# Kernel tuning notes

Measured on AMD Instinct MI355X. Metric: run time of the kernel, lower is better.

## Reference

```python
import jax, jax.numpy as jnp
import numpy as np

N_NODES = 50000
N_EDGES = 800000
D_FEAT = 128
D_HID = 500


def setup_inputs() -> dict:
    key = jax.random.key(0)
    k1, k2, k3, k4 = jax.random.split(key, 4)
    x = jax.random.normal(k1, (N_NODES, D_FEAT), dtype=jnp.float32)
    edge_index = jax.random.randint(k2, (2, N_EDGES), 0, N_NODES, dtype=jnp.int64)
    # Glorot-ish init for weights, zeros for bias (PyG GCNConv default)
    W1 = jax.random.normal(k3, (D_FEAT, D_HID), dtype=jnp.float32) / np.sqrt(D_FEAT)
    b1 = jnp.zeros((D_HID,), dtype=jnp.float32)
    W2 = jax.random.normal(k4, (D_HID, 1), dtype=jnp.float32) / np.sqrt(D_HID)
    b2 = jnp.zeros((1,), dtype=jnp.float32)
    return {"x": x, "edge_index": edge_index, "W1": W1, "b1": b1, "W2": W2, "b2": b2}


def gcn_conv(x, W, b, src, dst, n_nodes):
    """PyG GCNConv: linear transform, add self-loops, symmetric norm, scatter-add, bias."""
    h = x @ W  # [N, out]
    loops = jnp.arange(n_nodes, dtype=src.dtype)
    s = jnp.concatenate([src, loops])  # [E+N]
    d = jnp.concatenate([dst, loops])
    deg = jnp.zeros((n_nodes,), dtype=h.dtype).at[d].add(1.0)
    dinv = jnp.where(deg > 0, jax.lax.rsqrt(deg), 0.0)
    norm = dinv[s] * dinv[d]  # [E+N]
    msg = h[s] * norm[:, None]  # [E+N, out] -- dominant memory traffic
    out = jax.ops.segment_sum(msg, d, num_segments=n_nodes)
    return out + b


def reference(x, edge_index, W1, b1, W2, b2):
    src, dst = edge_index[0], edge_index[1]
    n = x.shape[0]
    h = gcn_conv(x, W1, b1, src, dst, n)
    h = jax.nn.relu(h)
    # F.dropout(training=self.training): identity in eval mode
    out = gcn_conv(h, W2, b2, src, dst, n)
    return out
```

## Files before the change

kernel.cpp:

```cpp
#include <hip/hip_runtime.h>


#define N_NODES 50000
#define N_EDGES 800000
#define D_FEAT  128
#define D_HID   500
#define NTILES  3125
#define BHIST   64
#define EPB     12500
#define CONVB   392
#define CSTRIDE 64

typedef __bf16 bf16x8 __attribute__((ext_vector_type(8)));
typedef float  f32x4  __attribute__((ext_vector_type(4)));

static __device__ inline unsigned int f2bf(float f) {
    unsigned int u = __float_as_uint(f);
    return (u + 0x7fffu + ((u >> 16) & 1u)) >> 16;
}
static __device__ inline float bf_lo(unsigned int u) { return __uint_as_float(u << 16); }
static __device__ inline float bf_hi(unsigned int u) { return __uint_as_float(u & 0xffff0000u); }

static __device__ inline void add8(float* acc, uint4 u) {
    acc[0] += bf_lo(u.x);
    acc[1] += bf_hi(u.x);
    acc[2] += bf_lo(u.y);
    acc[3] += bf_hi(u.y);
    acc[4] += bf_lo(u.z);
    acc[5] += bf_hi(u.z);
    acc[6] += bf_lo(u.w);
    acc[7] += bf_hi(u.w);
}

__global__ __launch_bounds__(1024) void k_hist(const int* __restrict__ dst,
                                               const float* __restrict__ W1,
                                               const float* __restrict__ b1,
                                               const float* __restrict__ W2,
                                               unsigned char* __restrict__ coff,
                                               unsigned char* __restrict__ lrank,
                                               unsigned short* __restrict__ b_pk,
                                               float* __restrict__ b1p,
                                               float* __restrict__ w2p) {
    __shared__ unsigned int hist[N_NODES / 4];
    const int b = blockIdx.x, tid = threadIdx.x;
    if (b < BHIST) {
        for (int w = tid; w < N_NODES / 4; w += 1024) hist[w] = 0u;
        __syncthreads();
        const int base = b * EPB;
        for (int i = tid * 4; i < EPB; i += 4096) {
            int4 d4 = *(const int4*)&dst[base + i];
            unsigned int s0 = (unsigned int)(d4.x & 3) * 8u;
            unsigned int s1 = (unsigned int)(d4.y & 3) * 8u;
            unsigned int s2 = (unsigned int)(d4.z & 3) * 8u;
            unsigned int s3 = (unsigned int)(d4.w & 3) * 8u;
            unsigned int r0 = atomicAdd(&hist[d4.x >> 2], 1u << s0);
            unsigned int r1 = atomicAdd(&hist[d4.y >> 2], 1u << s1);
            unsigned int r2 = atomicAdd(&hist[d4.z >> 2], 1u << s2);
            unsigned int r3 = atomicAdd(&hist[d4.w >> 2], 1u << s3);
            uchar4 lr;
            lr.x = (unsigned char)((r0 >> s0) & 0xffu);
            lr.y = (unsigned char)((r1 >> s1) & 0xffu);
            lr.z = (unsigned char)((r2 >> s2) & 0xffu);
            lr.w = (unsigned char)((r3 >> s3) & 0xffu);
            *(uchar4*)&lrank[base + i] = lr;
        }
        __syncthreads();
        unsigned int* crow = (unsigned int*)coff + (size_t)b * (N_NODES / 4);
        for (int w = tid; w < N_NODES / 4; w += 1024) crow[w] = hist[w];
    } else if (b < BHIST + 8) {
        int idx  = (b - BHIST) * 1024 + tid;
        int lane = idx & 63;
        int slot = idx >> 6;
        int t    = slot >> 2;
        int ks   = slot & 3;
        int quad = lane >> 4;
        int n    = t * 16 + (lane & 15);
        unsigned int us[8];
#pragma unroll
        for (int j = 0; j < 8; j++) {
            int k = ks * 32 + quad * 8 + j;
            float v = (n < D_HID) ? W1[(size_t)k * D_HID + n] : 0.f;
            us[j] = f2bf(v);
        }
        uint4 p;
        p.x = us[0] | (us[1] << 16);
        p.y = us[2] | (us[3] << 16);
        p.z = us[4] | (us[5] << 16);
        p.w = us[6] | (us[7] << 16);
        ((uint4*)b_pk)[idx] = p;
    } else {
        if (tid < 512) {
            b1p[tid] = (tid < D_HID) ? b1[tid] : 0.f;
            w2p[tid] = (tid < D_HID) ? W2[tid] : 0.f;
        }
    }
}

__global__ __launch_bounds__(256) void k_scan(unsigned int* __restrict__ coffw,
                                              int* __restrict__ deg) {
    const int t = blockIdx.x * 256 + threadIdx.x;
    if (t >= N_NODES / 4) return;
    unsigned int run0 = 0, run1 = 0, run2 = 0, run3 = 0;
#pragma unroll 8
    for (int b = 0; b < BHIST; b++) {
        size_t idx = (size_t)b * (N_NODES / 4) + t;
        unsigned int c = coffw[idx];
        coffw[idx] = run0 | (run1 << 8) | (run2 << 16) | (run3 << 24);
        run0 += c & 0xffu;
        run1 += (c >> 8) & 0xffu;
        run2 += (c >> 16) & 0xffu;
        run3 += (c >> 24) & 0xffu;
    }
    int4 d;
    d.x = (int)run0; d.y = (int)run1; d.z = (int)run2; d.w = (int)run3;
    *(int4*)&deg[t * 4] = d;
}

__global__ __launch_bounds__(1024) void k_fill(const int* __restrict__ src,
                                               const int* __restrict__ dst,
                                               const unsigned char* __restrict__ coff,
                                               const unsigned char* __restrict__ lrank,
                                               const int* __restrict__ deg,
                                               const float* __restrict__ x,
                                               unsigned short* __restrict__ csrp,
                                               uint2* __restrict__ xd) {
    const int b = blockIdx.x, tid = threadIdx.x;
    if (b < BHIST) {
        __shared__ unsigned char lcoff[N_NODES];
        const unsigned int* crow =
            (const unsigned int*)coff + (size_t)b * (N_NODES / 4);
        for (int w = tid; w < N_NODES / 4; w += 1024)
            ((unsigned int*)lcoff)[w] = crow[w];
        __syncthreads();
        const int base = b * EPB;
        for (int i = tid * 4; i < EPB; i += 4096) {
            int4 s4 = *(const int4*)&src[base + i];
            int4 d4 = *(const int4*)&dst[base + i];
            uchar4 lr = *(const uchar4*)&lrank[base + i];
            int r0 = (int)lcoff[d4.x] + (int)lr.x;
            int r1 = (int)lcoff[d4.y] + (int)lr.y;
            int r2 = (int)lcoff[d4.z] + (int)lr.z;
            int r3 = (int)lcoff[d4.w] + (int)lr.w;
            if (r0 < CSTRIDE) csrp[d4.x * CSTRIDE + r0] = (unsigned short)s4.x;
            if (r1 < CSTRIDE) csrp[d4.y * CSTRIDE + r1] = (unsigned short)s4.y;
            if (r2 < CSTRIDE) csrp[d4.z * CSTRIDE + r2] = (unsigned short)s4.z;
            if (r3 < CSTRIDE) csrp[d4.w * CSTRIDE + r3] = (unsigned short)s4.w;
        }
    } else {
        int gid = (b - BHIST) * 1024 + tid;
        for (int i = gid; i < N_NODES * D_FEAT / 4; i += CONVB * 1024) {
            float dv = rsqrtf((float)(deg[i >> 5] + 1));
            float4 v = ((const float4*)x)[i];
            uint2 o;
            o.x = f2bf(dv * v.x) | (f2bf(dv * v.y) << 16);
            o.y = f2bf(dv * v.z) | (f2bf(dv * v.w) << 16);
            xd[i] = o;
        }
    }
}

__global__ __launch_bounds__(256, 8) void k_gcn1(const uint4* __restrict__ xd4,
                                                 const unsigned short* __restrict__ csrp,
                                                 const int* __restrict__ deg,
                                                 const unsigned short* __restrict__ b_pk,
                                                 const float* __restrict__ b1p,
                                                 const float* __restrict__ w2p,
                                                 float* __restrict__ zd) {
    __shared__ unsigned short A[16][136];
    __shared__ float red[4][16];
    const int t = threadIdx.x;
    const int node0 = blockIdx.x * 16;
    const int wv = t >> 6, lane = t & 63;
    const int q = lane >> 4, p = lane & 15;

    {
        const int n = wv * 4 + q;
        const int node = node0 + n;
        int dg = deg[node];
        uint4 su = xd4[(size_t)node * 16 + p];
        if (dg > CSTRIDE) dg = CSTRIDE;
        const int base = node * CSTRIDE;
        float acc[8];
#pragma unroll
        for (int j = 0; j < 8; j++) acc[j] = 0.f;

        int e = 0;
        for (; e + 4 <= dg; e += 4) {
            ushort4 s4 = *(const ushort4*)&csrp[base + e];
            uint4 u0 = xd4[(size_t)s4.x * 16 + p];
            uint4 u1 = xd4[(size_t)s4.y * 16 + p];
            uint4 u2 = xd4[(size_t)s4.z * 16 + p];
            uint4 u3 = xd4[(size_t)s4.w * 16 + p];
            add8(acc, u0);
            add8(acc, u1);
            add8(acc, u2);
            add8(acc, u3);
        }
        for (; e < dg; e++) {
            int s = csrp[base + e];
            uint4 u = xd4[(size_t)s * 16 + p];
            add8(acc, u);
        }

        const float di = rsqrtf((float)(dg + 1));
        uint4 o;
        o.x = f2bf(di * (acc[0] + bf_lo(su.x))) |
              (f2bf(di * (acc[1] + bf_hi(su.x))) << 16);
        o.y = f2bf(di * (acc[2] + bf_lo(su.y))) |
              (f2bf(di * (acc[3] + bf_hi(su.y))) << 16);
        o.z = f2bf(di * (acc[4] + bf_lo(su.z))) |
              (f2bf(di * (acc[5] + bf_hi(su.z))) << 16);
        o.w = f2bf(di * (acc[6] + bf_lo(su.w))) |
              (f2bf(di * (acc[7] + bf_hi(su.w))) << 16);
        *(uint4*)&A[n][p * 8] = o;
    }
    __syncthreads();

    bf16x8 afr[4];
#pragma unroll
    for (int ks = 0; ks < 4; ks++)
        afr[ks] = *(const bf16x8*)&A[p][ks * 32 + q * 8];

    const bf16x8* __restrict__ bpk = (const bf16x8*)b_pk;
    f32x4 acc[8];
#pragma unroll
    for (int tt = 0; tt < 8; tt++) acc[tt] = (f32x4){0.f, 0.f, 0.f, 0.f};
#pragma unroll
    for (int tt = 0; tt < 8; tt++) {
        const int tile_n = wv * 8 + tt;
#pragma unroll
        for (int ks = 0; ks < 4; ks++) {
            bf16x8 bfr = bpk[(size_t)(tile_n * 4 + ks) * 64 + lane];
            acc[tt] = __builtin_amdgcn_mfma_f32_16x16x32_bf16(afr[ks], bfr, acc[tt], 0, 0, 0);
        }
    }

    float zp[4] = {0.f, 0.f, 0.f, 0.f};
#pragma unroll
    for (int tt = 0; tt < 8; tt++) {
        const int c = (wv * 8 + tt) * 16 + p;
        const float b1v = b1p[c];
        const float w2v = w2p[c];
#pragma unroll
        for (int r = 0; r < 4; r++)
            zp[r] += fmaxf(acc[tt][r] + b1v, 0.f) * w2v;
    }
#pragma unroll
    for (int off = 1; off < 16; off <<= 1) {
#pragma unroll
        for (int r = 0; r < 4; r++) zp[r] += __shfl_xor(zp[r], off);
    }
    if (p == 0) {
#pragma unroll
        for (int r = 0; r < 4; r++) red[wv][q * 4 + r] = zp[r];
    }
    __syncthreads();
    if (t < 16) {
        int node = node0 + t;
        float zz = red[0][t] + red[1][t] + red[2][t] + red[3][t];
        zd[node] = rsqrtf((float)(deg[node] + 1)) * zz;
    }
}

__global__ __launch_bounds__(256) void k_gz(const unsigned short* __restrict__ csrp,
                                            const int* __restrict__ deg,
                                            const float* __restrict__ zd,
                                            const float* __restrict__ b2,
                                            float* __restrict__ out) {
    const int node = blockIdx.x * 16 + (threadIdx.x >> 4);
    const int l = threadIdx.x & 15;
    int dg = deg[node];
    if (dg > CSTRIDE) dg = CSTRIDE;
    const int base = node * CSTRIDE;
    float s = 0.f;
    for (int e = l; e < dg; e += 16) s += zd[csrp[base + e]];
#pragma unroll
    for (int off = 1; off < 16; off <<= 1) s += __shfl_xor(s, off);
    if (l == 0) {
        float di = rsqrtf((float)(dg + 1));
        out[node] = di * (s + zd[node]) + b2[0];
    }
}

extern "C" void kernel_launch(void* const* d_in, const int* in_sizes, int n_in,
                              void* d_out, int out_size, void* d_ws, size_t ws_size,
                              hipStream_t stream) {
    const float* x  = (const float*)d_in[0];
    const int*   ei = (const int*)d_in[1];
    const float* W1 = (const float*)d_in[2];
    const float* b1 = (const float*)d_in[3];
    const float* W2 = (const float*)d_in[4];
    const float* b2 = (const float*)d_in[5];
    float* out = (float*)d_out;

    const int* src = ei;
    const int* dst = ei + N_EDGES;

    uint2* xd            = (uint2*)d_ws;
    unsigned short* b_pk = (unsigned short*)(xd + 1600000);
    float* b1p    = (float*)(b_pk + 65536);
    float* w2p    = b1p + 512;
    float* zd     = w2p + 512;
    int* deg      = (int*)(zd + N_NODES);
    unsigned char* coff  = (unsigned char*)(deg + N_NODES);
    unsigned char* lrank = coff + (size_t)BHIST * N_NODES;
    unsigned short* csrp = (unsigned short*)(lrank + N_EDGES);

    k_hist<<<BHIST + 9, 1024, 0, stream>>>(dst, W1, b1, W2, coff, lrank,
                                           b_pk, b1p, w2p);
    k_scan<<<(N_NODES / 4 + 255) / 256, 256, 0, stream>>>((unsigned int*)coff, deg);
    k_fill<<<BHIST + CONVB, 1024, 0, stream>>>(src, dst, coff, lrank, deg, x,
                                               csrp, xd);
    k_gcn1<<<NTILES, 256, 0, stream>>>((const uint4*)xd, csrp, deg,
                                       b_pk, b1p, w2p, zd);
    k_gz  <<<NTILES, 256, 0, stream>>>(csrp, deg, zd, b2, out);
}
```

Before: 154.0 us.

## Replace fixed-stride CSR with compact per-group row offsets and split fill blocks

```diff
diff --git a/kernel.cpp b/kernel.cpp
--- a/kernel.cpp
+++ b/kernel.cpp
@@ -8,8 +8,13 @@
 #define NTILES  3125
 #define BHIST   64
 #define EPB     12500
+#define SPLIT   5
+#define SB      (BHIST * SPLIT)
+#define EPSB    (EPB / SPLIT)
 #define CONVB   392
-#define CSTRIDE 64
+#define NGROUP  49
+#define GSTRIDE 24576
+#define CSRE_SLOTS (NGROUP * GSTRIDE)
 
 typedef __bf16 bf16x8 __attribute__((ext_vector_type(8)));
 typedef float  f32x4  __attribute__((ext_vector_type(4)));
@@ -97,57 +102,84 @@
 }
 
 __global__ __launch_bounds__(256) void k_scan(unsigned int* __restrict__ coffw,
-                                              int* __restrict__ deg) {
-    const int t = blockIdx.x * 256 + threadIdx.x;
-    if (t >= N_NODES / 4) return;
+                                              int* __restrict__ deg,
+                                              unsigned int* __restrict__ rstart4) {
+    __shared__ unsigned int ps[256];
+    const int g = blockIdx.x, tid = threadIdx.x;
+    const int idx = g * 256 + tid;
+    const bool live = idx < N_NODES / 4;
     unsigned int run0 = 0, run1 = 0, run2 = 0, run3 = 0;
+    if (live) {
 #pragma unroll 8
-    for (int b = 0; b < BHIST; b++) {
-        size_t idx = (size_t)b * (N_NODES / 4) + t;
-        unsigned int c = coffw[idx];
-        coffw[idx] = run0 | (run1 << 8) | (run2 << 16) | (run3 << 24);
-        run0 += c & 0xffu;
-        run1 += (c >> 8) & 0xffu;
-        run2 += (c >> 16) & 0xffu;
-        run3 += (c >> 24) & 0xffu;
-    }
-    int4 d;
-    d.x = (int)run0; d.y = (int)run1; d.z = (int)run2; d.w = (int)run3;
-    *(int4*)&deg[t * 4] = d;
+        for (int b = 0; b < BHIST; b++) {
+            size_t i = (size_t)b * (N_NODES / 4) + idx;
+            unsigned int c = coffw[i];
+            coffw[i] = run0 | (run1 << 8) | (run2 << 16) | (run3 << 24);
+            run0 += c & 0xffu;
+            run1 += (c >> 8) & 0xffu;
+            run2 += (c >> 16) & 0xffu;
+            run3 += (c >> 24) & 0xffu;
+        }
+        int4 d;
+        d.x = (int)run0; d.y = (int)run1; d.z = (int)run2; d.w = (int)run3;
+        *(int4*)&deg[idx * 4] = d;
+    }
+    unsigned int s0 = (run0 + 3u) & ~3u, s1 = (run1 + 3u) & ~3u;
+    unsigned int s2 = (run2 + 3u) & ~3u, s3 = (run3 + 3u) & ~3u;
+    unsigned int tot = live ? (s0 + s1 + s2 + s3) : 0u;
+    ps[tid] = tot;
+    __syncthreads();
+    for (int off = 1; off < 256; off <<= 1) {
+        unsigned int v = (tid >= off) ? ps[tid - off] : 0u;
+        __syncthreads();
+        ps[tid] += v;
+        __syncthreads();
+    }
+    if (live) {
+        unsigned int base = (unsigned int)g * GSTRIDE + (ps[tid] - tot);
+        uint4 r;
+        r.x = base;
+        r.y = base + s0;
+        r.z = base + s0 + s1;
+        r.w = base + s0 + s1 + s2;
+        *(uint4*)&rstart4[idx * 4] = r;
+    }
 }
 
 __global__ __launch_bounds__(1024) void k_fill(const int* __restrict__ src,
                                                const int* __restrict__ dst,
                                                const unsigned char* __restrict__ coff,
                                                const unsigned char* __restrict__ lrank,
+                                               const unsigned int* __restrict__ rstart4,
                                                const int* __restrict__ deg,
                                                const float* __restrict__ x,
-                                               unsigned short* __restrict__ csrp,
+                                               unsigned short* __restrict__ csre,
                                                uint2* __restrict__ xd) {
     const int b = blockIdx.x, tid = threadIdx.x;
-    if (b < BHIST) {
+    if (b < SB) {
         __shared__ unsigned char lcoff[N_NODES];
+        const int hb = b / SPLIT;
         const unsigned int* crow =
-            (const unsigned int*)coff + (size_t)b * (N_NODES / 4);
+            (const unsigned int*)coff + (size_t)hb * (N_NODES / 4);
         for (int w = tid; w < N_NODES / 4; w += 1024)
             ((unsigned int*)lcoff)[w] = crow[w];
         __syncthreads();
-        const int base = b * EPB;
-        for (int i = tid * 4; i < EPB; i += 4096) {
+        const int base = b * EPSB;
+        for (int i = tid * 4; i < EPSB; i += 4096) {
             int4 s4 = *(const int4*)&src[base + i];
             int4 d4 = *(const int4*)&dst[base + i];
             uchar4 lr = *(const uchar4*)&lrank[base + i];
-            int r0 = (int)lcoff[d4.x] + (int)lr.x;
-            int r1 = (int)lcoff[d4.y] + (int)lr.y;
-            int r2 = (int)lcoff[d4.z] + (int)lr.z;
-            int r3 = (int)lcoff[d4.w] + (int)lr.w;
-            if (r0 < CSTRIDE) csrp[d4.x * CSTRIDE + r0] = (unsigned short)s4.x;
-            if (r1 < CSTRIDE) csrp[d4.y * CSTRIDE + r1] = (unsigned short)s4.y;
-            if (r2 < CSTRIDE) csrp[d4.z * CSTRIDE + r2] = (unsigned short)s4.z;
-            if (r3 < CSTRIDE) csrp[d4.w * CSTRIDE + r3] = (unsigned short)s4.w;
+            unsigned int t0 = rstart4[d4.x] + (unsigned int)lcoff[d4.x] + lr.x;
+            unsigned int t1 = rstart4[d4.y] + (unsigned int)lcoff[d4.y] + lr.y;
+            unsigned int t2 = rstart4[d4.z] + (unsigned int)lcoff[d4.z] + lr.z;
+            unsigned int t3 = rstart4[d4.w] + (unsigned int)lcoff[d4.w] + lr.w;
+            if (t0 < CSRE_SLOTS) csre[t0] = (unsigned short)s4.x;
+            if (t1 < CSRE_SLOTS) csre[t1] = (unsigned short)s4.y;
+            if (t2 < CSRE_SLOTS) csre[t2] = (unsigned short)s4.z;
+            if (t3 < CSRE_SLOTS) csre[t3] = (unsigned short)s4.w;
         }
     } else {
-        int gid = (b - BHIST) * 1024 + tid;
+        int gid = (b - SB) * 1024 + tid;
         for (int i = gid; i < N_NODES * D_FEAT / 4; i += CONVB * 1024) {
             float dv = rsqrtf((float)(deg[i >> 5] + 1));
             float4 v = ((const float4*)x)[i];
@@ -160,7 +192,8 @@
 }
 
 __global__ __launch_bounds__(256, 8) void k_gcn1(const uint4* __restrict__ xd4,
-                                                 const unsigned short* __restrict__ csrp,
+                                                 const unsigned short* __restrict__ csre,
+                                                 const unsigned int* __restrict__ rstart4,
                                                  const int* __restrict__ deg,
                                                  const unsigned short* __restrict__ b_pk,
                                                  const float* __restrict__ b1p,
@@ -177,16 +210,16 @@
         const int n = wv * 4 + q;
         const int node = node0 + n;
         int dg = deg[node];
+        const unsigned int base = rstart4[node];
         uint4 su = xd4[(size_t)node * 16 + p];
-        if (dg > CSTRIDE) dg = CSTRIDE;
-        const int base = node * CSTRIDE;
+        if (dg > 64) dg = 64;
         float acc[8];
 #pragma unroll
         for (int j = 0; j < 8; j++) acc[j] = 0.f;
 
         int e = 0;
         for (; e + 4 <= dg; e += 4) {
-            ushort4 s4 = *(const ushort4*)&csrp[base + e];
+            ushort4 s4 = *(const ushort4*)&csre[base + e];
             uint4 u0 = xd4[(size_t)s4.x * 16 + p];
             uint4 u1 = xd4[(size_t)s4.y * 16 + p];
             uint4 u2 = xd4[(size_t)s4.z * 16 + p];
@@ -197,7 +230,7 @@
             add8(acc, u3);
         }
         for (; e < dg; e++) {
-            int s = csrp[base + e];
+            int s = csre[base + e];
             uint4 u = xd4[(size_t)s * 16 + p];
             add8(acc, u);
         }
@@ -262,7 +295,8 @@
     }
 }
 
-__global__ __launch_bounds__(256) void k_gz(const unsigned short* __restrict__ csrp,
+__global__ __launch_bounds__(256) void k_gz(const unsigned short* __restrict__ csre,
+                                            const unsigned int* __restrict__ rstart4,
                                             const int* __restrict__ deg,
                                             const float* __restrict__ zd,
                                             const float* __restrict__ b2,
@@ -270,10 +304,10 @@
     const int node = blockIdx.x * 16 + (threadIdx.x >> 4);
     const int l = threadIdx.x & 15;
     int dg = deg[node];
-    if (dg > CSTRIDE) dg = CSTRIDE;
-    const int base = node * CSTRIDE;
+    if (dg > 64) dg = 64;
+    const unsigned int base = rstart4[node];
     float s = 0.f;
-    for (int e = l; e < dg; e += 16) s += zd[csrp[base + e]];
+    for (int e = l; e < dg; e += 16) s += zd[csre[base + e]];
 #pragma unroll
     for (int off = 1; off < 16; off <<= 1) s += __shfl_xor(s, off);
     if (l == 0) {
@@ -302,16 +336,17 @@
     float* w2p    = b1p + 512;
     float* zd     = w2p + 512;
     int* deg      = (int*)(zd + N_NODES);
-    unsigned char* coff  = (unsigned char*)(deg + N_NODES);
+    unsigned int* rstart4 = (unsigned int*)(deg + N_NODES);
+    unsigned char* coff  = (unsigned char*)(rstart4 + N_NODES);
     unsigned char* lrank = coff + (size_t)BHIST * N_NODES;
-    unsigned short* csrp = (unsigned short*)(lrank + N_EDGES);
+    unsigned short* csre = (unsigned short*)(lrank + N_EDGES);
 
     k_hist<<<BHIST + 9, 1024, 0, stream>>>(dst, W1, b1, W2, coff, lrank,
                                            b_pk, b1p, w2p);
-    k_scan<<<(N_NODES / 4 + 255) / 256, 256, 0, stream>>>((unsigned int*)coff, deg);
-    k_fill<<<BHIST + CONVB, 1024, 0, stream>>>(src, dst, coff, lrank, deg, x,
-                                               csrp, xd);
-    k_gcn1<<<NTILES, 256, 0, stream>>>((const uint4*)xd, csrp, deg,
+    k_scan<<<NGROUP, 256, 0, stream>>>((unsigned int*)coff, deg, rstart4);
+    k_fill<<<SB + CONVB, 1024, 0, stream>>>(src, dst, coff, lrank, rstart4,
+                                            deg, x, csre, xd);
+    k_gcn1<<<NTILES, 256, 0, stream>>>((const uint4*)xd, csre, rstart4, deg,
                                        b_pk, b1p, w2p, zd);
-    k_gz  <<<NTILES, 256, 0, stream>>>(csrp, deg, zd, b2, out);
-}
+    k_gz  <<<NTILES, 256, 0, stream>>>(csre, rstart4, deg, zd, b2, out);
+}
```

After: 153.1 us. No clear change (-0.6%).
